# Optimization experiments

Hardware: AMD Instinct MI355X
Metric: run time of the kernel (lower is better)

## Reference

```python
import jax, jax.numpy as jnp
import numpy as np

N, E, FD, PD, C0, C1 = 50000, 1000000, 1024, 64, 64, 64


def setup_inputs() -> dict:
    key = jax.random.key(0)
    ks = iter(jax.random.split(key, 64))
    nrm = lambda s, sc=0.05: jax.random.normal(next(ks), s, jnp.float32) * sc

    def bn_p(c):
        # rows: gamma, beta, running_mean, running_var (eval-mode batchnorm)
        return jnp.stack([
            1.0 + 0.1 * jax.random.normal(next(ks), (c,)),
            0.1 * jax.random.normal(next(ks), (c,)),
            0.1 * jax.random.normal(next(ks), (c,)),
            0.5 + jax.random.uniform(next(ks), (c,)),
        ]).astype(jnp.float32)

    inp = {}
    inp["x"] = jax.random.normal(next(ks), (N, FD + 4), jnp.float32)
    inp["edge_index"] = jax.random.randint(next(ks), (2, E), 0, N, jnp.int32)
    inp["edge_attr"] = jax.random.randint(next(ks), (E,), 0, 3, jnp.int32) - 1  # {-1,0,1}
    inp["Wspf"] = nrm((PD, 4)); inp["bspf"] = nrm((PD,))
    inp["W011"] = nrm((C0, FD // 2 + PD)); inp["b011"] = nrm((C0,))
    inp["W012"] = nrm((C0, FD // 2)); inp["b012"] = nrm((C0,))
    inp["bn01"] = bn_p(C0)
    for i in (1, 2, 3):
        inp[f"e{i}W1"] = nrm((C0, 2 * C0)); inp[f"e{i}b1"] = nrm((C0,))
        inp[f"e{i}W2"] = nrm((C0, C0)); inp[f"e{i}b2"] = nrm((C0,))
        inp[f"bn1{i}"] = bn_p(C0)
    inp["s21Wl"] = nrm((C1, C0)); inp["s21bl"] = nrm((C1,)); inp["s21Wr"] = nrm((C1, C0))
    inp["bn21"] = bn_p(C1)
    for i in (1, 2, 3):
        inp[f"s3{i}Wl"] = nrm((1, C1)); inp[f"s3{i}bl"] = nrm((1,)); inp[f"s3{i}Wr"] = nrm((1, C1))
    return inp


def _bn(h, p):
    g, b, m, v = p
    return (h - m) * jax.lax.rsqrt(v + 1e-5) * g + b


def _edge_conv(h, src, dst, seg, n, W1, b1, W2, b2):
    # EdgeConv: max_j MLP([x_i, x_j - x_i]); masked edges routed to dummy segment n
    xi, xj = h[dst], h[src]
    msg = jax.nn.relu(jnp.concatenate([xi, xj - xi], axis=1) @ W1.T + b1) @ W2.T + b2
    out = jax.ops.segment_max(msg, seg, num_segments=n + 1)[:n]
    return jnp.where(jnp.isfinite(out), out, 0.0)  # nodes with no in-edges -> 0


def _sage(h, src, seg, n, Wl, bl, Wr):
    # SAGEConv: lin_l(mean_j x_j) + lin_r(x_i)
    s = jax.ops.segment_sum(h[src], seg, num_segments=n + 1)[:n]
    cnt = jax.ops.segment_sum(jnp.ones((seg.shape[0],), h.dtype), seg, num_segments=n + 1)[:n]
    agg = s / jnp.maximum(cnt, 1.0)[:, None]
    return agg @ Wl.T + bl + h @ Wr.T


def reference(x, edge_index, edge_attr, Wspf, bspf, W011, b011, W012, b012, bn01,
              e1W1, e1b1, e1W2, e1b2, bn11, e2W1, e2b1, e2W2, e2b2, bn12,
              e3W1, e3b1, e3W2, e3b2, bn13, s21Wl, s21bl, s21Wr, bn21,
              s31Wl, s31bl, s31Wr, s32Wl, s32bl, s32Wr, s33Wl, s33bl, s33Wr):
    fd = 1024
    n = x.shape[0]
    src, dst = edge_index[0], edge_index[1]
    seg1 = jnp.where(edge_attr >= 0, dst, n)  # forward-time edges
    seg2 = jnp.where(edge_attr <= 0, dst, n)  # backward-time edges
    seg3 = dst                                 # all edges

    spf = x[:, fd:fd + 4]
    x_vis = jnp.concatenate([x[:, fd // 2:fd], spf @ Wspf.T + bspf], axis=1) @ W011.T + b011
    x_aud = x[:, :fd // 2] @ W012.T + b012
    h = jax.nn.relu(_bn(x_aud + x_vis, bn01))

    def branch(eW1, eb1, eW2, eb2, bnE, seg, sWl, sbl, sWr):
        y = jax.nn.relu(_bn(_edge_conv(h, src, dst, seg, n, eW1, eb1, eW2, eb2), bnE))
        y = jax.nn.relu(_bn(_sage(y, src, seg, n, s21Wl, s21bl, s21Wr), bn21))
        return _sage(y, src, seg, n, sWl, sbl, sWr)

    o = (branch(e1W1, e1b1, e1W2, e1b2, bn11, seg1, s31Wl, s31bl, s31Wr)
         + branch(e2W1, e2b1, e2W2, e2b2, bn12, seg2, s32Wl, s32bl, s32Wr)
         + branch(e3W1, e3b1, e3W2, e3b2, bn13, seg3, s33Wl, s33bl, s33Wr))
    return jax.nn.sigmoid(o)
```

## Files before the change

kernel.cpp:

```cpp
#include <hip/hip_runtime.h>
#include <cstdint>
#include <cstddef>

#define NN 50000
#define EE 1000000
#define NBK 196
#define PWAVES 5120

typedef __attribute__((ext_vector_type(8))) short bf16x8;
typedef __attribute__((ext_vector_type(4))) short s16x4;
typedef __attribute__((ext_vector_type(4))) float f32x4;
typedef _Float16 f16;
typedef __attribute__((ext_vector_type(2))) _Float16 f16x2;
typedef __attribute__((ext_vector_type(4))) _Float16 f16x4;
typedef __attribute__((ext_vector_type(8))) _Float16 f16x8;

__device__ __forceinline__ void split2(float v, short& hi, short& lo) {
    union { float f; unsigned int u; } a; a.f = v;
    unsigned short h16 = (unsigned short)(a.u >> 16);
    union { unsigned int u; float f; } hf; hf.u = ((unsigned int)h16) << 16;
    union { float f; unsigned int u; } b; b.f = v - hf.f;
    hi = (short)h16;
    lo = (short)(b.u >> 16);
}

__device__ __forceinline__ f16x8 relupq(f16x8 p, f16x8 q) {
    f16x8 s = p + q;
    f16x8 z = {};
#if __has_builtin(__builtin_elementwise_max)
    return __builtin_elementwise_max(s, z);
#else
    f16x8 r;
#pragma unroll
    for (int j = 0; j < 8; j++) r[j] = (s[j] > (f16)0.f) ? s[j] : (f16)0.f;
    return r;
#endif
}

#define OFF_WHL    ((size_t)0)
#define OFF_WSPP   ((size_t)262144)
#define OFF_BIAS01 ((size_t)263168)
#define OFF_W1PQT  ((size_t)263424)
#define OFF_BIASPQ ((size_t)361728)
#define OFF_WSAGET ((size_t)363264)
#define OFF_BIAS21 ((size_t)396032)
#define OFF_BNF    ((size_t)396288)
#define OFF_W2BF   ((size_t)398848)
#define OFF_INVC4  ((size_t)423424)
#define OFF_PZ4    ((size_t)1223424)
#define OFF_RP     ((size_t)2023424)
#define OFF_PARTS  ((size_t)2223488)
#define OFF_DEG    ((size_t)2227584)
#define OFF_GHEAD  ((size_t)2427648)
#define OFF_SORT   ((size_t)2431744)
#define OFF_H      ((size_t)6431744)
#define OFF_PI     ((size_t)19231744)
#define OFF_QI     ((size_t)38431744)
#define OFF_Y1I    ((size_t)57631744)
#define OFF_EBUCK  OFF_H
#define OFF_AGGI   OFF_PI

__global__ __launch_bounds__(256) void k_prep(
    const float* __restrict__ Wspf, const float* __restrict__ bspf,
    const float* __restrict__ W011, const float* __restrict__ b011,
    const float* __restrict__ W012, const float* __restrict__ b012,
    const float* __restrict__ bn01,
    const float* __restrict__ e1W1, const float* __restrict__ e1b1,
    const float* __restrict__ e1b2, const float* __restrict__ bn11,
    const float* __restrict__ e2W1, const float* __restrict__ e2b1,
    const float* __restrict__ e2b2, const float* __restrict__ bn12,
    const float* __restrict__ e3W1, const float* __restrict__ e3b1,
    const float* __restrict__ e3b2, const float* __restrict__ bn13,
    const float* __restrict__ e1W2, const float* __restrict__ e2W2,
    const float* __restrict__ e3W2,
    const float* __restrict__ s21Wl, const float* __restrict__ s21bl,
    const float* __restrict__ s21Wr, const float* __restrict__ bn21,
    unsigned short* __restrict__ Whl, float* __restrict__ WspP, float* __restrict__ bias01,
    float* __restrict__ W1pqT, float* __restrict__ biasPQ,
    float* __restrict__ WsageT, float* __restrict__ bias21, float* __restrict__ bnf,
    f16* __restrict__ W2h)
{
    int idx = blockIdx.x * 256 + threadIdx.x;
    if (idx < 131072) {
        int hl = idx >> 16;
        int r = idx & 65535;
        int kchunk = r >> 11;
        int r2 = r & 2047;
        int blk = r2 >> 9;
        int r3 = r2 & 511;
        int lane = r3 >> 3;
        int j = r3 & 7;
        int n = lane & 15, quad = lane >> 4;
        int k = kchunk * 32 + quad * 8 + j;
        int c = blk * 16 + n;
        float s = bn01[c] * rsqrtf(bn01[192 + c] + 1e-5f);
        float w = ((k < 512) ? W012[c * 512 + k] : W011[c * 576 + (k - 512)]) * s;
        short hi, lo;
        split2(w, hi, lo);
        Whl[idx] = (unsigned short)(hl ? lo : hi);
    } else if (idx < 131072 + 24576) {
        int r = idx - 131072;
        int b = r >> 13; r &= 8191;
        int k = r >> 7, cp = r & 127;
        const float* W1 = (b == 0) ? e1W1 : (b == 1) ? e2W1 : e3W1;
        float val;
        if (cp < 64) val = W1[cp * 128 + k] - W1[cp * 128 + 64 + k];
        else         val = W1[(cp - 64) * 128 + 64 + k];
        W1pqT[b * 8192 + k * 128 + cp] = val;
    } else if (idx < 131072 + 24576 + 8192) {
        int r = idx - (131072 + 24576);
        int k = r >> 6, c = r & 63;
        float s = bn21[c] * rsqrtf(bn21[192 + c] + 1e-5f);
        float w = (k < 64) ? s21Wl[c * 64 + k] : s21Wr[c * 64 + (k - 64)];
        WsageT[k * 64 + c] = w * s;
    } else if (idx < 131072 + 24576 + 8192 + 64) {
        int c = idx - (131072 + 24576 + 8192);
        float s01 = bn01[c] * rsqrtf(bn01[192 + c] + 1e-5f);
        float wsp0 = 0.f, wsp1 = 0.f, wsp2 = 0.f, wsp3 = 0.f, bacc = 0.f;
        for (int j = 0; j < 64; j++) {
            float w = W011[c * 576 + 512 + j];
            wsp0 += w * Wspf[j * 4 + 0];
            wsp1 += w * Wspf[j * 4 + 1];
            wsp2 += w * Wspf[j * 4 + 2];
            wsp3 += w * Wspf[j * 4 + 3];
            bacc += w * bspf[j];
        }
        WspP[c * 4 + 0] = wsp0 * s01; WspP[c * 4 + 1] = wsp1 * s01;
        WspP[c * 4 + 2] = wsp2 * s01; WspP[c * 4 + 3] = wsp3 * s01;
        bias01[c] = (b011[c] + b012[c] + bacc) * s01 + (bn01[64 + c] - bn01[128 + c] * s01);
        float s21 = bn21[c] * rsqrtf(bn21[192 + c] + 1e-5f);
        bias21[c] = s21bl[c] * s21 + (bn21[64 + c] - bn21[128 + c] * s21);
        const float* b1a[3] = { e1b1, e2b1, e3b1 };
        const float* b2a[3] = { e1b2, e2b2, e3b2 };
        const float* bna[3] = { bn11, bn12, bn13 };
#pragma unroll
        for (int b = 0; b < 3; b++) {
            float s = bna[b][c] * rsqrtf(bna[b][192 + c] + 1e-5f);
            float tr = bna[b][64 + c] - bna[b][128 + c] * s;
            bnf[b * 192 + c] = s;
            bnf[b * 192 + 64 + c] = b2a[b][c] * s + tr;
            bnf[b * 192 + 128 + c] = tr;
            biasPQ[b * 128 + c] = b1a[b][c];
            biasPQ[b * 128 + 64 + c] = 0.f;
        }
    } else if (idx < 131072 + 24576 + 8192 + 64 + 12288) {
        int r = idx - (131072 + 24576 + 8192 + 64);
        int b = r >> 12, i = r & 4095;
        const float* W2 = (b == 0) ? e1W2 : (b == 1) ? e2W2 : e3W2;
        W2h[b * 4096 + i] = (f16)W2[i];
    }
}

__global__ __launch_bounds__(256) void k_hist(
    const int* __restrict__ dst, int* __restrict__ deg)
{
    int e = blockIdx.x * 256 + threadIdx.x;
    if (e < EE) atomicAdd(&deg[dst[e]], 1);
}

__global__ __launch_bounds__(256) void k_psum(const int* __restrict__ deg, int* __restrict__ parts)
{
    int i = blockIdx.x * 256 + threadIdx.x;
    int v = (i < NN) ? deg[i] : 0;
#pragma unroll
    for (int off = 32; off > 0; off >>= 1) v += __shfl_xor(v, off);
    __shared__ int ws4[4];
    int wid = threadIdx.x >> 6;
    if ((threadIdx.x & 63) == 0) ws4[wid] = v;
    __syncthreads();
    if (threadIdx.x == 0)
        parts[blockIdx.x] = ws4[0] + ws4[1] + ws4[2] + ws4[3];
}

__global__ __launch_bounds__(256) void k_pscan(int* __restrict__ parts)
{
    __shared__ int sbuf[256];
    int tid = threadIdx.x;
    int v = (tid < NBK) ? parts[tid] : 0;
    sbuf[tid] = v;
    __syncthreads();
    for (int off = 1; off < 256; off <<= 1) {
        int t = (tid >= off) ? sbuf[tid - off] : 0;
        __syncthreads();
        sbuf[tid] += t;
        __syncthreads();
    }
    if (tid < NBK) parts[tid] = sbuf[tid] - v;
}

__global__ __launch_bounds__(256) void k_scanfix(
    const int* __restrict__ deg, const int* __restrict__ parts, int* __restrict__ rowptr)
{
    __shared__ int sbuf[256];
    int tid = threadIdx.x;
    int i = blockIdx.x * 256 + tid;
    int v = (i < NN) ? deg[i] : 0;
    sbuf[tid] = v;
    __syncthreads();
    for (int off = 1; off < 256; off <<= 1) {
        int t = (tid >= off) ? sbuf[tid - off] : 0;
        __syncthreads();
        sbuf[tid] += t;
        __syncthreads();
    }
    int base = parts[blockIdx.x];
    if (i < NN)      rowptr[i] = base + sbuf[tid] - v;
    if (i == NN - 1) rowptr[NN] = base + sbuf[tid];
}

__global__ __launch_bounds__(256) void k_gheadinit(
    const int* __restrict__ rp, int* __restrict__ ghead)
{
    int t = threadIdx.x;
    if (t < NBK) ghead[t] = rp[t * 256];
}

__global__ __launch_bounds__(256) void k_bucketA(
    const int* __restrict__ src, const int* __restrict__ dst, const int* __restrict__ attr,
    int* __restrict__ ghead, unsigned int* __restrict__ ebuck)
{
    __shared__ int hist[NBK];
    __shared__ int head[NBK];
    int tid = threadIdx.x;
    if (tid < NBK) hist[tid] = 0;
    __syncthreads();
    int base_e = blockIdx.x * 4096;
    unsigned int word[16]; int bkt[16];
#pragma unroll
    for (int k = 0; k < 16; k++) {
        int e = base_e + k * 256 + tid;
        if (e < EE) {
            int d = dst[e], s = src[e], a = attr[e] + 1;
            int b = d >> 8;
            word[k] = (unsigned)s | ((unsigned)a << 16) | ((unsigned)(d & 255) << 18);
            bkt[k] = b;
            atomicAdd(&hist[b], 1);
        } else { bkt[k] = -1; word[k] = 0; }
    }
    __syncthreads();
    if (tid < NBK) {
        int c = hist[tid];
        head[tid] = c ? atomicAdd(&ghead[tid], c) : 0;
    }
    __syncthreads();
#pragma unroll
    for (int k = 0; k < 16; k++) {
        if (bkt[k] >= 0) {
            int pos = atomicAdd(&head[bkt[k]], 1);
            ebuck[pos] = word[k];
        }
    }
}

__global__ __launch_bounds__(256) void k_bucketB(
    const int* __restrict__ rp, const unsigned int* __restrict__ ebuck,
    int* __restrict__ sorted)
{
    __shared__ int sbuf[256];
    __shared__ int head[256];
    int b = blockIdx.x, tid = threadIdx.x;
    int n0 = b * 256;
    int n1 = n0 + 256; if (n1 > NN) n1 = NN;
    int r0 = rp[n0];
    int r1 = rp[n1];
    sbuf[tid] = 0;
    __syncthreads();
    for (int e = r0 + tid; e < r1; e += 256)
        atomicAdd(&sbuf[(ebuck[e] >> 18) & 255], 1);
    __syncthreads();
    int v = sbuf[tid];
    for (int off = 1; off < 256; off <<= 1) {
        int t = (tid >= off) ? sbuf[tid - off] : 0;
        __syncthreads();
        sbuf[tid] += t;
        __syncthreads();
    }
    head[tid] = r0 + sbuf[tid] - v;
    __syncthreads();
    for (int e = r0 + tid; e < r1; e += 256) {
        unsigned int w = ebuck[e];
        int pos = atomicAdd(&head[(w >> 18) & 255], 1);
        sorted[pos] = (int)(w & 0x3FFFFu);
    }
}

__global__ __launch_bounds__(256) void k_h(
    const float* __restrict__ x, const unsigned short* __restrict__ Whl,
    const float* __restrict__ WspP, const float* __restrict__ bias01,
    float* __restrict__ h)
{
    __shared__ unsigned short hib[2][4096];
    __shared__ unsigned short lob[2][4096];
    int tid = threadIdx.x;
    int w = tid >> 6, l = tid & 63;
    int tile = blockIdx.x;
    int m = l & 15, quad = l >> 4;
    int blk = w;
    const unsigned short* Wh = Whl;
    const unsigned short* Wl = Whl + 65536;
    const size_t xbase = (size_t)tile * 16 * 1028;

    int oct_w = l >> 1, off_w = (l & 1) * 4;

    f32x4 g[4];
#pragma unroll
    for (int p = 0; p < 4; p++)
        g[p] = *(const f32x4*)(x + xbase + (size_t)(p * 4 + w) * 1028 + l * 4);
#pragma unroll
    for (int p = 0; p < 4; p++) {
        int r = p * 4 + w;
        int op = r * 256 + (oct_w ^ (r & 7)) * 8 + off_w;
        s16x4 h4, l4;
#pragma unroll
        for (int i = 0; i < 4; i++) { short hi, lo; split2(g[p][i], hi, lo); h4[i] = hi; l4[i] = lo; }
        *(s16x4*)(&hib[0][op]) = h4;
        *(s16x4*)(&lob[0][op]) = l4;
    }
    __syncthreads();

    f32x4 acc = { 0.f, 0.f, 0.f, 0.f };
    for (int c = 0; c < 4; c++) {
        if (c < 3) {
#pragma unroll
            for (int p = 0; p < 4; p++)
                g[p] = *(const f32x4*)(x + xbase + (size_t)(p * 4 + w) * 1028 + (c + 1) * 256 + l * 4);
        }
        int buf = c & 1;
        const unsigned short* hp = &hib[buf][m * 256];
        const unsigned short* lp = &lob[buf][m * 256];
        int msw = m & 7;
#pragma unroll
        for (int ks = 0; ks < 8; ks++) {
            int oct = ks * 4 + quad;
            int ao = (oct ^ msw) * 8;
            bf16x8 xh = *(const bf16x8*)(hp + ao);
            bf16x8 xl = *(const bf16x8*)(lp + ao);
            int fb = (c * 8 + ks) * 2048 + blk * 512 + l * 8;
            bf16x8 bh = *(const bf16x8*)(Wh + fb);
            bf16x8 bl = *(const bf16x8*)(Wl + fb);
            acc = __builtin_amdgcn_mfma_f32_16x16x32_bf16(xh, bh, acc, 0, 0, 0);
            acc = __builtin_amdgcn_mfma_f32_16x16x32_bf16(xl, bh, acc, 0, 0, 0);
            acc = __builtin_amdgcn_mfma_f32_16x16x32_bf16(xh, bl, acc, 0, 0, 0);
        }
        if (c < 3) {
            int nbuf = (c + 1) & 1;
#pragma unroll
            for (int p = 0; p < 4; p++) {
                int r = p * 4 + w;
                int op = r * 256 + (oct_w ^ (r & 7)) * 8 + off_w;
                s16x4 h4, l4;
#pragma unroll
                for (int i = 0; i < 4; i++) { short hi, lo; split2(g[p][i], hi, lo); h4[i] = hi; l4[i] = lo; }
                *(s16x4*)(&hib[nbuf][op]) = h4;
                *(s16x4*)(&lob[nbuf][op]) = l4;
            }
            __syncthreads();
        }
    }

    int ch = blk * 16 + m;
    f32x4 wsp = *(const f32x4*)(WspP + ch * 4);
    float bia = bias01[ch];
#pragma unroll
    for (int r = 0; r < 4; r++) {
        int row = tile * 16 + quad * 4 + r;
        f32x4 sp = *(const f32x4*)(x + (size_t)row * 1028 + 1024);
        float a = acc[r] + sp[0] * wsp[0] + sp[1] * wsp[1]
                + sp[2] * wsp[2] + sp[3] * wsp[3] + bia;
        h[(size_t)row * 64 + ch] = fmaxf(a, 0.f);
    }
}

__global__ __launch_bounds__(256) void k_pq(
    const float* __restrict__ h, const float* __restrict__ WT3,
    const float* __restrict__ biasPQ, f16* __restrict__ Pi, f16* __restrict__ Qi)
{
    __shared__ float wt[64 * 128];
    __shared__ float xt[64 * 68];
    int tid = threadIdx.x;
    int m0 = blockIdx.x * 64;
    int cg = tid & 31, rg = tid >> 5;
#pragma unroll
    for (int i = 0; i < 4; i++) {
        int li = i * 256 + tid;
        int rr = li >> 4, q = li & 15;
        int row = m0 + rr;
        float4 u = make_float4(0.f, 0.f, 0.f, 0.f);
        if (row < NN) u = *(const float4*)(h + (size_t)row * 64 + q * 4);
        *(float4*)(xt + rr * 68 + q * 4) = u;
    }
    for (int b = 0; b < 3; b++) {
        __syncthreads();
#pragma unroll
        for (int i = 0; i < 8; i++)
            ((float4*)wt)[i * 256 + tid] = ((const float4*)(WT3 + b * 8192))[i * 256 + tid];
        __syncthreads();
        float acc[8][4];
#pragma unroll
        for (int r = 0; r < 8; r++)
#pragma unroll
            for (int j = 0; j < 4; j++) acc[r][j] = 0.f;
#pragma unroll 8
        for (int k = 0; k < 64; k++) {
            float4 wv = *(const float4*)(wt + k * 128 + cg * 4);
#pragma unroll
            for (int r = 0; r < 8; r++) {
                float xv = xt[(rg * 8 + r) * 68 + k];
                acc[r][0] += xv * wv.x; acc[r][1] += xv * wv.y;
                acc[r][2] += xv * wv.z; acc[r][3] += xv * wv.w;
            }
        }
        const float* biasP = biasPQ + b * 128;
#pragma unroll
        for (int r = 0; r < 8; r++) {
            int row = m0 + rg * 8 + r;
            if (row < NN) {
                if (cg < 16) {
                    f16x4 res;
#pragma unroll
                    for (int j = 0; j < 4; j++)
                        res[j] = (f16)(acc[r][j] + biasP[cg * 4 + j]);
                    *(f16x4*)(Pi + (size_t)row * 192 + b * 64 + cg * 4) = res;
                } else {
                    f16x4 res;
#pragma unroll
                    for (int j = 0; j < 4; j++)
                        res[j] = (f16)acc[r][j];
                    *(f16x4*)(Qi + (size_t)row * 192 + b * 64 + (cg - 16) * 4) = res;
                }
            }
        }
    }
}

#define ECV_LDS_BRANCH(B, PL, PH, Q0, Q1, MASK, ACC)                               \
    if ((MASK) & 0xFFFFull) {                                                      \
        f16x8 a0 = relupq(PL, Q0);                                                 \
        f16x8 a1 = relupq(PH, Q1);                                                 \
        _Pragma("unroll") for (int blk = 0; blk < 4; blk++) {                      \
            f32x4 c = { 0.f, 0.f, 0.f, 0.f };                                      \
            f16x8 w0 = *(const f16x8*)(w2s + ((B) * 8 + blk * 2 + 0) * 512 + quad * 128 + m * 8); \
            f16x8 w1 = *(const f16x8*)(w2s + ((B) * 8 + blk * 2 + 1) * 512 + quad * 128 + m * 8); \
            c = __builtin_amdgcn_mfma_f32_16x16x32_f16(a0, w0, c, 0, 0, 0);        \
            c = __builtin_amdgcn_mfma_f32_16x16x32_f16(a1, w1, c, 0, 0, 0);        \
            _Pragma("unroll") for (int r = 0; r < 4; r++)                          \
                if (((MASK) >> (vsh + r)) & 1)                                     \
                    ACC[blk][r] = fmaxf(ACC[blk][r], c[r]);                        \
        }                                                                          \
    }

#define ECV_EPI(B, ACC, CNT)                                                       \
    {                                                                              \
        float red[4];                                                              \
        _Pragma("unroll") for (int blk = 0; blk < 4; blk++) {                      \
            float rv = fmaxf(fmaxf(ACC[blk][0], ACC[blk][1]),                      \
                             fmaxf(ACC[blk][2], ACC[blk][3]));                     \
            rv = fmaxf(rv, __shfl_xor(rv, 16));                                    \
            rv = fmaxf(rv, __shfl_xor(rv, 32));                                    \
            red[blk] = rv;                                                         \
        }                                                                          \
        float mx = red[quad];                                                      \
        const float* scb = bnf + (B) * 192;                                        \
        float outv = ((CNT) > 0) ? fmaxf(fmaf(mx, scb[lane], scb[64 + lane]), 0.f) \
                                 : fmaxf(scb[128 + lane], 0.f);                    \
        y1i[(size_t)v * 192 + (B) * 64 + lane] = (f16)outv;                        \
    }

__global__ __launch_bounds__(256) void k_edgeconv_f(
    const int* __restrict__ rowptr, const int* __restrict__ sorted,
    const f16* __restrict__ Pi, const f16* __restrict__ Qi,
    const f16* __restrict__ W2h,
    const float* __restrict__ bnf,
    f16* __restrict__ y1i, float* __restrict__ invc4)
{
    __shared__ f16 w2s[12288];
    int tid = threadIdx.x;
#pragma unroll
    for (int u0 = 0; u0 < 6; u0++) {
        int u = u0 * 256 + tid;
        int frag = u >> 6;
        int rem = u & 63;
        int m2 = rem >> 2, qd = rem & 3;
        int bb = frag >> 3, blk = (frag >> 1) & 3, kc = frag & 1;
        *(int4*)(w2s + frag * 512 + qd * 128 + m2 * 8) =
            *(const int4*)(W2h + (bb * 64 + blk * 16 + m2) * 64 + kc * 32 + qd * 8);
    }
    __syncthreads();

    int wid = tid >> 6, lane = tid & 63;
    int m = lane & 15, quad = lane >> 4;
    int gw = blockIdx.x * 4 + wid;

    for (int v = gw; v < NN; v += PWAVES) {
        const f16* pr = Pi + (size_t)v * 192;
        f16x8 pl0 = *(const f16x8*)(pr + 0   + quad * 8);
        f16x8 ph0 = *(const f16x8*)(pr + 32  + quad * 8);
        f16x8 pl1 = *(const f16x8*)(pr + 64  + quad * 8);
        f16x8 ph1 = *(const f16x8*)(pr + 96  + quad * 8);
        f16x8 pl2 = *(const f16x8*)(pr + 128 + quad * 8);
        f16x8 ph2 = *(const f16x8*)(pr + 160 + quad * 8);

        int e0 = rowptr[v], e1 = rowptr[v + 1];
        int deg = e1 - e0;
        float acc0[4][4], acc1[4][4], acc2[4][4];
#pragma unroll
        for (int blk = 0; blk < 4; blk++)
#pragma unroll
            for (int r = 0; r < 4; r++) {
                acc0[blk][r] = -3.0e38f; acc1[blk][r] = -3.0e38f; acc2[blk][r] = -3.0e38f;
            }

        int cnt1 = 0, cnt2 = 0;
        int vsh = quad * 4;
        int nb = (deg + 15) >> 4;
        for (int bi = 0; bi < nb; bi++) {
            int e = e0 + bi * 16 + m;
            bool in = e < e1;
            int wrd = in ? sorted[e] : 0;
            int srcm = in ? (wrd & 0xFFFF) : v;
            int a = (wrd >> 16) & 3;
            bool mm1 = in && (a >= 1);
            bool mm2 = in && (a <= 1);
            const f16* qr = Qi + (size_t)srcm * 192;
            f16x8 q30 = *(const f16x8*)(qr + 128 + quad * 8);
            f16x8 q31 = *(const f16x8*)(qr + 160 + quad * 8);
            f16x8 q10 = {}, q11 = {}, q20 = {}, q21 = {};
            if (mm1) { q10 = *(const f16x8*)(qr + quad * 8);      q11 = *(const f16x8*)(qr + 32 + quad * 8); }
            if (mm2) { q20 = *(const f16x8*)(qr + 64 + quad * 8); q21 = *(const f16x8*)(qr + 96 + quad * 8); }
            unsigned long long bl1 = __ballot(mm1);
            unsigned long long bl2 = __ballot(mm2);
            unsigned long long bl3 = __ballot(in);
            cnt1 += __popc((unsigned)bl1 & 0xFFFFu);
            cnt2 += __popc((unsigned)bl2 & 0xFFFFu);

            ECV_LDS_BRANCH(2, pl2, ph2, q30, q31, bl3, acc2)
            ECV_LDS_BRANCH(0, pl0, ph0, q10, q11, bl1, acc0)
            ECV_LDS_BRANCH(1, pl1, ph1, q20, q21, bl2, acc1)
        }

        ECV_EPI(0, acc0, cnt1)
        ECV_EPI(1, acc1, cnt2)
        ECV_EPI(2, acc2, deg)
        if (lane == 0) {
            float4 ic;
            ic.x = 1.f / (float)(cnt1 > 0 ? cnt1 : 1);
            ic.y = 1.f / (float)(cnt2 > 0 ? cnt2 : 1);
            ic.z = 1.f / (float)(deg  > 0 ? deg  : 1);
            ic.w = 0.f;
            *(float4*)(invc4 + (size_t)v * 4) = ic;
        }
    }
}

__global__ __launch_bounds__(256) void k_agg_f(
    const int* __restrict__ rowptr, const int* __restrict__ sorted,
    const f16* __restrict__ y1i, const float* __restrict__ invc4,
    f16* __restrict__ aggi)
{
    int wid = threadIdx.x >> 6, lane = threadIdx.x & 63;
    int eslot = lane >> 3, cg = lane & 7;
    int gw = blockIdx.x * 4 + wid;
    for (int v = gw; v < NN; v += PWAVES) {
        int e0 = rowptr[v], e1 = rowptr[v + 1];
        float s1[8], s2[8], s3[8];
#pragma unroll
        for (int j = 0; j < 8; j++) { s1[j] = 0.f; s2[j] = 0.f; s3[j] = 0.f; }
        for (int eb = e0; eb < e1; eb += 8) {
            int e = eb + eslot;
            bool val = e < e1;
            int ec = val ? e : (e1 - 1);
            int w = sorted[ec];
            int src = w & 0xFFFF, a = (w >> 16) & 3;
            float f3 = val ? 1.f : 0.f;
            float f1 = (val && a >= 1) ? 1.f : 0.f;
            float f2 = (val && a <= 1) ? 1.f : 0.f;
            const f16* row = y1i + (size_t)src * 192 + cg * 8;
            f16x8 u1 = *(const f16x8*)(row);
            f16x8 u2 = *(const f16x8*)(row + 64);
            f16x8 u3 = *(const f16x8*)(row + 128);
#pragma unroll
            for (int j = 0; j < 8; j++) {
                s1[j] = fmaf(f1, (float)u1[j], s1[j]);
                s2[j] = fmaf(f2, (float)u2[j], s2[j]);
                s3[j] = fmaf(f3, (float)u3[j], s3[j]);
            }
        }
#pragma unroll
        for (int j = 0; j < 8; j++) {
            s1[j] += __shfl_xor(s1[j], 8);  s1[j] += __shfl_xor(s1[j], 16); s1[j] += __shfl_xor(s1[j], 32);
            s2[j] += __shfl_xor(s2[j], 8);  s2[j] += __shfl_xor(s2[j], 16); s2[j] += __shfl_xor(s2[j], 32);
            s3[j] += __shfl_xor(s3[j], 8);  s3[j] += __shfl_xor(s3[j], 16); s3[j] += __shfl_xor(s3[j], 32);
        }
        if (eslot == 0) {
            float4 icv = *(const float4*)(invc4 + (size_t)v * 4);
            f16* od = aggi + (size_t)v * 192 + cg * 8;
            f16x8 r1, r2, r3;
#pragma unroll
            for (int j = 0; j < 8; j++) {
                r1[j] = (f16)(s1[j] * icv.x);
                r2[j] = (f16)(s2[j] * icv.y);
                r3[j] = (f16)(s3[j] * icv.z);
            }
            *(f16x8*)(od)       = r1;
            *(f16x8*)(od + 64)  = r2;
            *(f16x8*)(od + 128) = r3;
        }
    }
}

__global__ __launch_bounds__(256) void k_sage1(
    const f16* __restrict__ aggA, const f16* __restrict__ y1A,
    const float* __restrict__ WsageT, const float* __restrict__ bias21,
    const float* __restrict__ Wl3, const float* __restrict__ bl3,
    const float* __restrict__ Wr3,
    float* __restrict__ pz4, int b)
{
    __shared__ float wt[64 * 64];
    __shared__ float xt[128 * 68];
    __shared__ float wl[64], wr[64];
    int tid = threadIdx.x;
    int m0 = blockIdx.x * 128;
    int cg = tid & 15, rg = tid >> 4;
    if (tid < 64) { wl[tid] = Wl3[tid]; wr[tid] = Wr3[tid]; }
    float blv = bl3[0];
    float acc[8][4];
#pragma unroll
    for (int r = 0; r < 8; r++)
#pragma unroll
        for (int j = 0; j < 4; j++) acc[r][j] = 0.f;
    for (int ch = 0; ch < 2; ch++) {
        const f16* A = ch ? y1A : aggA;
        __syncthreads();
#pragma unroll
        for (int i = 0; i < 4; i++)
            ((float4*)wt)[i * 256 + tid] = ((const float4*)(WsageT + ch * 4096))[i * 256 + tid];
#pragma unroll
        for (int i = 0; i < 4; i++) {
            int li = i * 256 + tid;
            int rr = li >> 3, q = li & 7;
            int row = m0 + rr;
            f16x8 u = {};
            if (row < NN) u = *(const f16x8*)(A + (size_t)row * 192 + q * 8);
            float4 lo4 = make_float4((float)u[0], (float)u[1], (float)u[2], (float)u[3]);
            float4 hi4 = make_float4((float)u[4], (float)u[5], (float)u[6], (float)u[7]);
            *(float4*)(xt + rr * 68 + q * 8) = lo4;
            *(float4*)(xt + rr * 68 + q * 8 + 4) = hi4;
        }
        __syncthreads();
#pragma unroll 8
        for (int k = 0; k < 64; k++) {
            float4 wv = *(const float4*)(wt + k * 64 + cg * 4);
#pragma unroll
            for (int r = 0; r < 8; r++) {
                float xv = xt[(rg * 8 + r) * 68 + k];
                acc[r][0] += xv * wv.x; acc[r][1] += xv * wv.y;
                acc[r][2] += xv * wv.z; acc[r][3] += xv * wv.w;
            }
        }
    }
#pragma unroll
    for (int r = 0; r < 8; r++) {
        int row = m0 + rg * 8 + r;
        float ap = 0.f, az = 0.f;
#pragma unroll
        for (int j = 0; j < 4; j++) {
            float t = fmaxf(acc[r][j] + bias21[cg * 4 + j], 0.f);
            ap += t * wl[cg * 4 + j];
            az += t * wr[cg * 4 + j];
        }
        ap += __shfl_xor(ap, 1); ap += __shfl_xor(ap, 2);
        ap += __shfl_xor(ap, 4); ap += __shfl_xor(ap, 8);
        az += __shfl_xor(az, 1); az += __shfl_xor(az, 2);
        az += __shfl_xor(az, 4); az += __shfl_xor(az, 8);
        if (cg == 0 && row < NN) {
            pz4[(size_t)row * 4 + b] = ap;
            float zz = az + blv;
            if (b == 0) pz4[(size_t)row * 4 + 3] = zz;
            else        pz4[(size_t)row * 4 + 3] += zz;
        }
    }
}

__global__ __launch_bounds__(256) void k_sage2_f(
    const int* __restrict__ rowptr, const int* __restrict__ sorted,
    const float* __restrict__ pz4, const float* __restrict__ invc4,
    float* __restrict__ outp)
{
    int wid = threadIdx.x >> 6, lane = threadIdx.x & 63;
    int gw = blockIdx.x * 4 + wid;
    for (int v = gw; v < NN; v += PWAVES) {
        int e0 = rowptr[v], e1 = rowptr[v + 1];
        float s1 = 0.f, s2 = 0.f, s3 = 0.f;
        for (int e = e0 + lane; e < e1; e += 64) {
            int w = sorted[e];
            int src = w & 0xFFFF, a = (w >> 16) & 3;
            float4 pz = *(const float4*)(pz4 + (size_t)src * 4);
            s3 += pz.z;
            if (a >= 1) s1 += pz.x;
            if (a <= 1) s2 += pz.y;
        }
#pragma unroll
        for (int off = 32; off > 0; off >>= 1) {
            s1 += __shfl_xor(s1, off);
            s2 += __shfl_xor(s2, off);
            s3 += __shfl_xor(s3, off);
        }
        if (lane == 0) {
            float4 icv = *(const float4*)(invc4 + (size_t)v * 4);
            float zsum = pz4[(size_t)v * 4 + 3];
            float val = s1 * icv.x + s2 * icv.y + s3 * icv.z + zsum;
            outp[v] = 1.f / (1.f + expf(-val));
        }
    }
}

extern "C" void kernel_launch(void* const* d_in, const int* in_sizes, int n_in,
                              void* d_out, int out_size, void* d_ws, size_t ws_size,
                              hipStream_t stream)
{
    const float* x    = (const float*)d_in[0];
    const int* ei     = (const int*)d_in[1];
    const int* attr   = (const int*)d_in[2];
    const float* Wspf = (const float*)d_in[3];
    const float* bspf = (const float*)d_in[4];
    const float* W011 = (const float*)d_in[5];
    const float* b011 = (const float*)d_in[6];
    const float* W012 = (const float*)d_in[7];
    const float* b012 = (const float*)d_in[8];
    const float* bn01 = (const float*)d_in[9];
    const float* eW1[3] = { (const float*)d_in[10], (const float*)d_in[15], (const float*)d_in[20] };
    const float* eb1[3] = { (const float*)d_in[11], (const float*)d_in[16], (const float*)d_in[21] };
    const float* eW2[3] = { (const float*)d_in[12], (const float*)d_in[17], (const float*)d_in[22] };
    const float* eb2[3] = { (const float*)d_in[13], (const float*)d_in[18], (const float*)d_in[23] };
    const float* bn1[3] = { (const float*)d_in[14], (const float*)d_in[19], (const float*)d_in[24] };
    const float* s21Wl = (const float*)d_in[25];
    const float* s21bl = (const float*)d_in[26];
    const float* s21Wr = (const float*)d_in[27];
    const float* bn21  = (const float*)d_in[28];
    const float* s3Wl[3] = { (const float*)d_in[29], (const float*)d_in[32], (const float*)d_in[35] };
    const float* s3bl[3] = { (const float*)d_in[30], (const float*)d_in[33], (const float*)d_in[36] };
    const float* s3Wr[3] = { (const float*)d_in[31], (const float*)d_in[34], (const float*)d_in[37] };

    char* ws = (char*)d_ws;
    unsigned short* Whl = (unsigned short*)(ws + OFF_WHL);
    float* WspP   = (float*)(ws + OFF_WSPP);
    float* bias01 = (float*)(ws + OFF_BIAS01);
    float* W1pqT  = (float*)(ws + OFF_W1PQT);
    float* biasPQ = (float*)(ws + OFF_BIASPQ);
    float* WsageT = (float*)(ws + OFF_WSAGET);
    float* bias21 = (float*)(ws + OFF_BIAS21);
    float* bnf    = (float*)(ws + OFF_BNF);
    f16*   W2h    = (f16*)(ws + OFF_W2BF);
    float* invc4  = (float*)(ws + OFF_INVC4);
    float* pz4    = (float*)(ws + OFF_PZ4);
    int*   rp     = (int*)(ws + OFF_RP);
    int*   parts  = (int*)(ws + OFF_PARTS);
    int*   deg    = (int*)(ws + OFF_DEG);
    int*   ghead  = (int*)(ws + OFF_GHEAD);
    int*   sorted = (int*)(ws + OFF_SORT);
    unsigned int* ebuck = (unsigned int*)(ws + OFF_EBUCK);
    float* h      = (float*)(ws + OFF_H);
    f16*   Pi     = (f16*)(ws + OFF_PI);
    f16*   Qi     = (f16*)(ws + OFF_QI);
    f16*   y1i    = (f16*)(ws + OFF_Y1I);
    f16*   aggi   = (f16*)(ws + OFF_AGGI);

    hipMemsetAsync(ws + OFF_DEG, 0, 200064, stream);

    k_prep<<<689, 256, 0, stream>>>(
        Wspf, bspf, W011, b011, W012, b012, bn01,
        eW1[0], eb1[0], eb2[0], bn1[0],
        eW1[1], eb1[1], eb2[1], bn1[1],
        eW1[2], eb1[2], eb2[2], bn1[2],
        eW2[0], eW2[1], eW2[2],
        s21Wl, s21bl, s21Wr, bn21,
        Whl, WspP, bias01, W1pqT, biasPQ, WsageT, bias21, bnf, W2h);

    k_hist<<<3907, 256, 0, stream>>>(ei + EE, deg);
    k_psum<<<NBK, 256, 0, stream>>>(deg, parts);
    k_pscan<<<1, 256, 0, stream>>>(parts);
    k_scanfix<<<NBK, 256, 0, stream>>>(deg, parts, rp);
    k_gheadinit<<<1, 256, 0, stream>>>(rp, ghead);
    k_bucketA<<<245, 256, 0, stream>>>(ei, ei + EE, attr, ghead, ebuck);
    k_bucketB<<<NBK, 256, 0, stream>>>(rp, ebuck, sorted);

    k_h<<<3125, 256, 0, stream>>>(x, Whl, WspP, bias01, h);

    k_pq<<<782, 256, 0, stream>>>(h, W1pqT, biasPQ, Pi, Qi);

    k_edgeconv_f<<<PWAVES / 4, 256, 0, stream>>>(rp, sorted, Pi, Qi, W2h, bnf, y1i, invc4);
    k_agg_f<<<PWAVES / 4, 256, 0, stream>>>(rp, sorted, y1i, invc4, aggi);

    for (int b = 0; b < 3; b++)
        k_sage1<<<391, 256, 0, stream>>>(aggi + b * 64, y1i + b * 64, WsageT, bias21,
                                         s3Wl[b], s3bl[b], s3Wr[b], pz4, b);

    k_sage2_f<<<PWAVES / 4, 256, 0, stream>>>(rp, sorted, pz4, invc4, (float*)d_out);
}
```

Before: 770.2 us.

## Merge sage1 launches, drop gheadinit, specialize edge tails, retune wave counts

Several changes at once. The three per-branch k_sage1 launches are merged into one kernel that loops over branches and accumulates the z term in registers instead of doing a read-modify-write on pz4. The bucket heads are now written directly by k_pscan, which removes the k_gheadinit launch. In edgeconv, the all-edges branch skips per-row masking on full 16-edge blocks, and k_agg_f skips invalid or masked edges instead of multiplying by zero flags. Persistent-wave counts also rise for the edgeconv and aggregation kernels. Risks are added branch divergence and register pressure.

```diff
diff --git a/kernel.cpp b/kernel.cpp
--- a/kernel.cpp
+++ b/kernel.cpp
@@ -5,7 +5,8 @@
 #define NN 50000
 #define EE 1000000
 #define NBK 196
-#define PWAVES 5120
+#define PW_EC 6144
+#define PW_AG 8192
 
 typedef __attribute__((ext_vector_type(8))) short bf16x8;
 typedef __attribute__((ext_vector_type(4))) short s16x4;
@@ -172,7 +173,7 @@
         parts[blockIdx.x] = ws4[0] + ws4[1] + ws4[2] + ws4[3];
 }
 
-__global__ __launch_bounds__(256) void k_pscan(int* __restrict__ parts)
+__global__ __launch_bounds__(256) void k_pscan(int* __restrict__ parts, int* __restrict__ ghead)
 {
     __shared__ int sbuf[256];
     int tid = threadIdx.x;
@@ -185,7 +186,11 @@
         sbuf[tid] += t;
         __syncthreads();
     }
-    if (tid < NBK) parts[tid] = sbuf[tid] - v;
+    if (tid < NBK) {
+        int ex = sbuf[tid] - v;
+        parts[tid] = ex;
+        ghead[tid] = ex;
+    }
 }
 
 __global__ __launch_bounds__(256) void k_scanfix(
@@ -206,13 +211,6 @@
     int base = parts[blockIdx.x];
     if (i < NN)      rowptr[i] = base + sbuf[tid] - v;
     if (i == NN - 1) rowptr[NN] = base + sbuf[tid];
-}
-
-__global__ __launch_bounds__(256) void k_gheadinit(
-    const int* __restrict__ rp, int* __restrict__ ghead)
-{
-    int t = threadIdx.x;
-    if (t < NBK) ghead[t] = rp[t * 256];
 }
 
 __global__ __launch_bounds__(256) void k_bucketA(
@@ -491,7 +489,7 @@
     int m = lane & 15, quad = lane >> 4;
     int gw = blockIdx.x * 4 + wid;
 
-    for (int v = gw; v < NN; v += PWAVES) {
+    for (int v = gw; v < NN; v += PW_EC) {
         const f16* pr = Pi + (size_t)v * 192;
         f16x8 pl0 = *(const f16x8*)(pr + 0   + quad * 8);
         f16x8 ph0 = *(const f16x8*)(pr + 32  + quad * 8);
@@ -513,14 +511,16 @@
         int cnt1 = 0, cnt2 = 0;
         int vsh = quad * 4;
         int nb = (deg + 15) >> 4;
+        bool hastail = (deg & 15) != 0;
         for (int bi = 0; bi < nb; bi++) {
+            bool tailb = hastail && (bi == nb - 1);
             int e = e0 + bi * 16 + m;
-            bool in = e < e1;
-            int wrd = in ? sorted[e] : 0;
-            int srcm = in ? (wrd & 0xFFFF) : v;
+            bool inn = tailb ? (e < e1) : true;
+            int wrd = inn ? sorted[e] : 0;
+            int srcm = inn ? (wrd & 0xFFFF) : v;
             int a = (wrd >> 16) & 3;
-            bool mm1 = in && (a >= 1);
-            bool mm2 = in && (a <= 1);
+            bool mm1 = inn && (a >= 1);
+            bool mm2 = inn && (a <= 1);
             const f16* qr = Qi + (size_t)srcm * 192;
             f16x8 q30 = *(const f16x8*)(qr + 128 + quad * 8);
             f16x8 q31 = *(const f16x8*)(qr + 160 + quad * 8);
@@ -529,11 +529,40 @@
             if (mm2) { q20 = *(const f16x8*)(qr + 64 + quad * 8); q21 = *(const f16x8*)(qr + 96 + quad * 8); }
             unsigned long long bl1 = __ballot(mm1);
             unsigned long long bl2 = __ballot(mm2);
-            unsigned long long bl3 = __ballot(in);
             cnt1 += __popc((unsigned)bl1 & 0xFFFFu);
             cnt2 += __popc((unsigned)bl2 & 0xFFFFu);
 
-            ECV_LDS_BRANCH(2, pl2, ph2, q30, q31, bl3, acc2)
+            {
+                f16x8 a30 = relupq(pl2, q30);
+                f16x8 a31 = relupq(ph2, q31);
+                if (!tailb) {
+#pragma unroll
+                    for (int blk = 0; blk < 4; blk++) {
+                        f32x4 c = { 0.f, 0.f, 0.f, 0.f };
+                        f16x8 w0 = *(const f16x8*)(w2s + (16 + blk * 2 + 0) * 512 + quad * 128 + m * 8);
+                        f16x8 w1 = *(const f16x8*)(w2s + (16 + blk * 2 + 1) * 512 + quad * 128 + m * 8);
+                        c = __builtin_amdgcn_mfma_f32_16x16x32_f16(a30, w0, c, 0, 0, 0);
+                        c = __builtin_amdgcn_mfma_f32_16x16x32_f16(a31, w1, c, 0, 0, 0);
+#pragma unroll
+                        for (int r = 0; r < 4; r++)
+                            acc2[blk][r] = fmaxf(acc2[blk][r], c[r]);
+                    }
+                } else {
+                    unsigned long long bl3 = __ballot(inn);
+#pragma unroll
+                    for (int blk = 0; blk < 4; blk++) {
+                        f32x4 c = { 0.f, 0.f, 0.f, 0.f };
+                        f16x8 w0 = *(const f16x8*)(w2s + (16 + blk * 2 + 0) * 512 + quad * 128 + m * 8);
+                        f16x8 w1 = *(const f16x8*)(w2s + (16 + blk * 2 + 1) * 512 + quad * 128 + m * 8);
+                        c = __builtin_amdgcn_mfma_f32_16x16x32_f16(a30, w0, c, 0, 0, 0);
+                        c = __builtin_amdgcn_mfma_f32_16x16x32_f16(a31, w1, c, 0, 0, 0);
+#pragma unroll
+                        for (int r = 0; r < 4; r++)
+                            if ((bl3 >> (vsh + r)) & 1)
+                                acc2[blk][r] = fmaxf(acc2[blk][r], c[r]);
+                    }
+                }
+            }
             ECV_LDS_BRANCH(0, pl0, ph0, q10, q11, bl1, acc0)
             ECV_LDS_BRANCH(1, pl1, ph1, q20, q21, bl2, acc1)
         }
@@ -560,29 +589,30 @@
     int wid = threadIdx.x >> 6, lane = threadIdx.x & 63;
     int eslot = lane >> 3, cg = lane & 7;
     int gw = blockIdx.x * 4 + wid;
-    for (int v = gw; v < NN; v += PWAVES) {
+    for (int v = gw; v < NN; v += PW_AG) {
         int e0 = rowptr[v], e1 = rowptr[v + 1];
         float s1[8], s2[8], s3[8];
 #pragma unroll
         for (int j = 0; j < 8; j++) { s1[j] = 0.f; s2[j] = 0.f; s3[j] = 0.f; }
         for (int eb = e0; eb < e1; eb += 8) {
             int e = eb + eslot;
-            bool val = e < e1;
-            int ec = val ? e : (e1 - 1);
-            int w = sorted[ec];
-            int src = w & 0xFFFF, a = (w >> 16) & 3;
-            float f3 = val ? 1.f : 0.f;
-            float f1 = (val && a >= 1) ? 1.f : 0.f;
-            float f2 = (val && a <= 1) ? 1.f : 0.f;
-            const f16* row = y1i + (size_t)src * 192 + cg * 8;
-            f16x8 u1 = *(const f16x8*)(row);
-            f16x8 u2 = *(const f16x8*)(row + 64);
-            f16x8 u3 = *(const f16x8*)(row + 128);
-#pragma unroll
-            for (int j = 0; j < 8; j++) {
-                s1[j] = fmaf(f1, (float)u1[j], s1[j]);
-                s2[j] = fmaf(f2, (float)u2[j], s2[j]);
-                s3[j] = fmaf(f3, (float)u3[j], s3[j]);
+            if (e < e1) {
+                int w = sorted[e];
+                int src = w & 0xFFFF, a = (w >> 16) & 3;
+                const f16* row = y1i + (size_t)src * 192 + cg * 8;
+                f16x8 u3 = *(const f16x8*)(row + 128);
+#pragma unroll
+                for (int j = 0; j < 8; j++) s3[j] += (float)u3[j];
+                if (a >= 1) {
+                    f16x8 u1 = *(const f16x8*)(row);
+#pragma unroll
+                    for (int j = 0; j < 8; j++) s1[j] += (float)u1[j];
+                }
+                if (a <= 1) {
+                    f16x8 u2 = *(const f16x8*)(row + 64);
+#pragma unroll
+                    for (int j = 0; j < 8; j++) s2[j] += (float)u2[j];
+                }
             }
         }
 #pragma unroll
@@ -609,11 +639,12 @@
 }
 
 __global__ __launch_bounds__(256) void k_sage1(
-    const f16* __restrict__ aggA, const f16* __restrict__ y1A,
+    const f16* __restrict__ aggi, const f16* __restrict__ y1i,
     const float* __restrict__ WsageT, const float* __restrict__ bias21,
-    const float* __restrict__ Wl3, const float* __restrict__ bl3,
-    const float* __restrict__ Wr3,
-    float* __restrict__ pz4, int b)
+    const float* __restrict__ Wl0, const float* __restrict__ bl0, const float* __restrict__ Wr0,
+    const float* __restrict__ Wl1, const float* __restrict__ bl1, const float* __restrict__ Wr1,
+    const float* __restrict__ Wl2, const float* __restrict__ bl2, const float* __restrict__ Wr2,
+    float* __restrict__ pz4)
 {
     __shared__ float wt[64 * 64];
     __shared__ float xt[128 * 68];
@@ -621,63 +652,76 @@
     int tid = threadIdx.x;
     int m0 = blockIdx.x * 128;
     int cg = tid & 15, rg = tid >> 4;
-    if (tid < 64) { wl[tid] = Wl3[tid]; wr[tid] = Wr3[tid]; }
-    float blv = bl3[0];
-    float acc[8][4];
-#pragma unroll
-    for (int r = 0; r < 8; r++)
-#pragma unroll
-        for (int j = 0; j < 4; j++) acc[r][j] = 0.f;
-    for (int ch = 0; ch < 2; ch++) {
-        const f16* A = ch ? y1A : aggA;
+    float zsum[8];
+#pragma unroll
+    for (int r = 0; r < 8; r++) zsum[r] = 0.f;
+
+    for (int b = 0; b < 3; b++) {
+        const float* Wl3 = (b == 0) ? Wl0 : (b == 1) ? Wl1 : Wl2;
+        const float* bl3 = (b == 0) ? bl0 : (b == 1) ? bl1 : bl2;
+        const float* Wr3 = (b == 0) ? Wr0 : (b == 1) ? Wr1 : Wr2;
         __syncthreads();
-#pragma unroll
-        for (int i = 0; i < 4; i++)
-            ((float4*)wt)[i * 256 + tid] = ((const float4*)(WsageT + ch * 4096))[i * 256 + tid];
-#pragma unroll
-        for (int i = 0; i < 4; i++) {
-            int li = i * 256 + tid;
-            int rr = li >> 3, q = li & 7;
-            int row = m0 + rr;
-            f16x8 u = {};
-            if (row < NN) u = *(const f16x8*)(A + (size_t)row * 192 + q * 8);
-            float4 lo4 = make_float4((float)u[0], (float)u[1], (float)u[2], (float)u[3]);
-            float4 hi4 = make_float4((float)u[4], (float)u[5], (float)u[6], (float)u[7]);
-            *(float4*)(xt + rr * 68 + q * 8) = lo4;
-            *(float4*)(xt + rr * 68 + q * 8 + 4) = hi4;
-        }
-        __syncthreads();
+        if (tid < 64) { wl[tid] = Wl3[tid]; wr[tid] = Wr3[tid]; }
+        float blv = bl3[0];
+        float acc[8][4];
+#pragma unroll
+        for (int r = 0; r < 8; r++)
+#pragma unroll
+            for (int j = 0; j < 4; j++) acc[r][j] = 0.f;
+        for (int ch = 0; ch < 2; ch++) {
+            const f16* A = (ch ? y1i : aggi) + b * 64;
+            __syncthreads();
+#pragma unroll
+            for (int i = 0; i < 4; i++)
+                ((float4*)wt)[i * 256 + tid] = ((const float4*)(WsageT + ch * 4096))[i * 256 + tid];
+#pragma unroll
+            for (int i = 0; i < 4; i++) {
+                int li = i * 256 + tid;
+                int rr = li >> 3, q = li & 7;
+                int row = m0 + rr;
+                f16x8 u = {};
+                if (row < NN) u = *(const f16x8*)(A + (size_t)row * 192 + q * 8);
+                float4 lo4 = make_float4((float)u[0], (float)u[1], (float)u[2], (float)u[3]);
+                float4 hi4 = make_float4((float)u[4], (float)u[5], (float)u[6], (float)u[7]);
+                *(float4*)(xt + rr * 68 + q * 8) = lo4;
+                *(float4*)(xt + rr * 68 + q * 8 + 4) = hi4;
+            }
+            __syncthreads();
 #pragma unroll 8
-        for (int k = 0; k < 64; k++) {
-            float4 wv = *(const float4*)(wt + k * 64 + cg * 4);
-#pragma unroll
-            for (int r = 0; r < 8; r++) {
-                float xv = xt[(rg * 8 + r) * 68 + k];
-                acc[r][0] += xv * wv.x; acc[r][1] += xv * wv.y;
-                acc[r][2] += xv * wv.z; acc[r][3] += xv * wv.w;
-            }
+            for (int k = 0; k < 64; k++) {
+                float4 wv = *(const float4*)(wt + k * 64 + cg * 4);
+#pragma unroll
+                for (int r = 0; r < 8; r++) {
+                    float xv = xt[(rg * 8 + r) * 68 + k];
+                    acc[r][0] += xv * wv.x; acc[r][1] += xv * wv.y;
+                    acc[r][2] += xv * wv.z; acc[r][3] += xv * wv.w;
+                }
+            }
+        }
+#pragma unroll
+        for (int r = 0; r < 8; r++) {
+            int row = m0 + rg * 8 + r;
+            float ap = 0.f, az = 0.f;
+#pragma unroll
+            for (int j = 0; j < 4; j++) {
+                float t = fmaxf(acc[r][j] + bias21[cg * 4 + j], 0.f);
+                ap += t * wl[cg * 4 + j];
+                az += t * wr[cg * 4 + j];
+            }
+            ap += __shfl_xor(ap, 1); ap += __shfl_xor(ap, 2);
+            ap += __shfl_xor(ap, 4); ap += __shfl_xor(ap, 8);
+            az += __shfl_xor(az, 1); az += __shfl_xor(az, 2);
+            az += __shfl_xor(az, 4); az += __shfl_xor(az, 8);
+            zsum[r] += az + blv;
+            if (cg == 0 && row < NN)
+                pz4[(size_t)row * 4 + b] = ap;
         }
     }
 #pragma unroll
     for (int r = 0; r < 8; r++) {
         int row = m0 + rg * 8 + r;
-        float ap = 0.f, az = 0.f;
-#pragma unroll
-        for (int j = 0; j < 4; j++) {
-            float t = fmaxf(acc[r][j] + bias21[cg * 4 + j], 0.f);
-            ap += t * wl[cg * 4 + j];
-            az += t * wr[cg * 4 + j];
-        }
-        ap += __shfl_xor(ap, 1); ap += __shfl_xor(ap, 2);
-        ap += __shfl_xor(ap, 4); ap += __shfl_xor(ap, 8);
-        az += __shfl_xor(az, 1); az += __shfl_xor(az, 2);
-        az += __shfl_xor(az, 4); az += __shfl_xor(az, 8);
-        if (cg == 0 && row < NN) {
-            pz4[(size_t)row * 4 + b] = ap;
-            float zz = az + blv;
-            if (b == 0) pz4[(size_t)row * 4 + 3] = zz;
-            else        pz4[(size_t)row * 4 + 3] += zz;
-        }
+        if (cg == 0 && row < NN)
+            pz4[(size_t)row * 4 + 3] = zsum[r];
     }
 }
 
@@ -688,7 +732,7 @@
 {
     int wid = threadIdx.x >> 6, lane = threadIdx.x & 63;
     int gw = blockIdx.x * 4 + wid;
-    for (int v = gw; v < NN; v += PWAVES) {
+    for (int v = gw; v < NN; v += PW_AG) {
         int e0 = rowptr[v], e1 = rowptr[v + 1];
         float s1 = 0.f, s2 = 0.f, s3 = 0.f;
         for (int e = e0 + lane; e < e1; e += 64) {
@@ -778,9 +822,8 @@
 
     k_hist<<<3907, 256, 0, stream>>>(ei + EE, deg);
     k_psum<<<NBK, 256, 0, stream>>>(deg, parts);
-    k_pscan<<<1, 256, 0, stream>>>(parts);
+    k_pscan<<<1, 256, 0, stream>>>(parts, ghead);
     k_scanfix<<<NBK, 256, 0, stream>>>(deg, parts, rp);
-    k_gheadinit<<<1, 256, 0, stream>>>(rp, ghead);
     k_bucketA<<<245, 256, 0, stream>>>(ei, ei + EE, attr, ghead, ebuck);
     k_bucketB<<<NBK, 256, 0, stream>>>(rp, ebuck, sorted);
 
@@ -788,12 +831,13 @@
 
     k_pq<<<782, 256, 0, stream>>>(h, W1pqT, biasPQ, Pi, Qi);
 
-    k_edgeconv_f<<<PWAVES / 4, 256, 0, stream>>>(rp, sorted, Pi, Qi, W2h, bnf, y1i, invc4);
-    k_agg_f<<<PWAVES / 4, 256, 0, stream>>>(rp, sorted, y1i, invc4, aggi);
-
-    for (int b = 0; b < 3; b++)
-        k_sage1<<<391, 256, 0, stream>>>(aggi + b * 64, y1i + b * 64, WsageT, bias21,
-                                         s3Wl[b], s3bl[b], s3Wr[b], pz4, b);
-
-    k_sage2_f<<<PWAVES / 4, 256, 0, stream>>>(rp, sorted, pz4, invc4, (float*)d_out);
-}
+    k_edgeconv_f<<<PW_EC / 4, 256, 0, stream>>>(rp, sorted, Pi, Qi, W2h, bnf, y1i, invc4);
+    k_agg_f<<<PW_AG / 4, 256, 0, stream>>>(rp, sorted, y1i, invc4, aggi);
+
+    k_sage1<<<391, 256, 0, stream>>>(aggi, y1i, WsageT, bias21,
+                                     s3Wl[0], s3bl[0], s3Wr[0],
+                                     s3Wl[1], s3bl[1], s3Wr[1],
+                                     s3Wl[2], s3bl[2], s3Wr[2], pz4);
+
+    k_sage2_f<<<PW_AG / 4, 256, 0, stream>>>(rp, sorted, pz4, invc4, (float*)d_out);
+}
```

New measurement: 757.9 us. No clear change (-1.6%).
